# Kernel tuning notes

Measured on AMD Instinct MI355X. Metric: run time of the kernel, lower is better.

## Reference

```python
import jax, jax.numpy as jnp
import numpy as np


def setup_inputs() -> dict:
    key = jax.random.key(0)
    ks = jax.random.split(key, 6)
    B, S, T, E, D = 16, 128, 128, 512, 512  # batch, enc steps, dec steps, enc units, dec units
    scale = 0.05
    return {
        "enc": jax.random.normal(ks[0], (B, S, E), dtype=jnp.float32),
        "dec": jax.random.normal(ks[1], (B, T, D), dtype=jnp.float32),
        "W1": jax.random.normal(ks[2], (E, E), dtype=jnp.float32) * scale,
        "W2": jax.random.normal(ks[3], (D, E), dtype=jnp.float32) * scale,
        "b": jax.random.normal(ks[4], (1, 1, E), dtype=jnp.float32) * scale,
        "V": jax.random.normal(ks[5], (E, 1), dtype=jnp.float32) * scale,
    }


def reference(enc, dec, W1, W2, b, V):
    # Vectorized Bahdanau additive attention (the original loops over decoder
    # timesteps with keras.backend.rnn; the steps are independent so we batch them).
    W1_hs = jnp.einsum('bse,ef->bsf', enc, W1)            # [B,S,E] (computed once, not per step)
    W2_ht = jnp.einsum('btd,de->bte', dec, W2)            # [B,T,E]
    # tanh(W1.hs + W2.ht + b): broadcast to [B,T,S,E]
    scores = jnp.tanh(W1_hs[:, None, :, :] + W2_ht[:, :, None, :] + b)
    logits = jnp.einsum('btse,e->bts', scores, V[:, 0])   # [B,T,S]
    attn_weights = jax.nn.softmax(logits, axis=-1)        # softmax over encoder steps
    context_vectors = jnp.einsum('bts,bse->bte', attn_weights, enc)  # [B,T,E]
    return (context_vectors, attn_weights)
```

## Files before the change

kernel.cpp:

```cpp
#include <hip/hip_runtime.h>
#include <hip/hip_bf16.h>
#include <cstddef>


constexpr int nBt = 16, nSq = 128, nTq = 128, nEd = 512;

typedef __attribute__((ext_vector_type(4))) float f32x4;
typedef __attribute__((ext_vector_type(8))) short s16x8;

#define PRESCALE 2.8853900817779268f
#define LOG2E 1.4426950408889634f

__device__ __forceinline__ unsigned short to_bf(float f) {
    unsigned u = __builtin_bit_cast(unsigned, f);
    return (unsigned short)((u + 0x7FFFu + ((u >> 16) & 1u)) >> 16);
}
__device__ __forceinline__ float from_bf(unsigned short h) {
    unsigned u = ((unsigned)h) << 16;
    return __builtin_bit_cast(float, u);
}

__global__ __launch_bounds__(256) void kWprep(
    const float* __restrict__ W1, const float* __restrict__ W2,
    unsigned short* __restrict__ WT)
{
    const int z = blockIdx.z;
    const float* W = z ? W2 : W1;
    __shared__ float tl[32][33];
    const int r  = threadIdx.x >> 3;
    const int c4 = (threadIdx.x & 7) * 4;
    const int kB = blockIdx.y * 32;
    const int nB = blockIdx.x * 32;
    const float4 v = *(const float4*)&W[(size_t)(kB + r) * nEd + nB + c4];
    tl[r][c4 + 0] = v.x; tl[r][c4 + 1] = v.y;
    tl[r][c4 + 2] = v.z; tl[r][c4 + 3] = v.w;
    __syncthreads();
    unsigned short hh[4], ll[4];
    #pragma unroll
    for (int i = 0; i < 4; ++i) {
        const float x = tl[c4 + i][r];
        hh[i] = to_bf(x);
        ll[i] = to_bf(x - from_bf(hh[i]));
    }
    const size_t o = ((size_t)z * nEd + nB + r) * nEd + kB + c4;
    *(ushort4*)&WT[o] = *(ushort4*)hh;
    *(ushort4*)&WT[(size_t)2 * nEd * nEd + o] = *(ushort4*)ll;
}

__global__ __launch_bounds__(256) void kMgemmB(
    const float* __restrict__ A0, const float* __restrict__ A1,
    const unsigned short* __restrict__ WT, const float* __restrict__ bias,
    float* __restrict__ C0, float* __restrict__ C1)
{
    const int z = blockIdx.z;
    const float* __restrict__ A = z ? A1 : A0;
    const unsigned short* __restrict__ Wh = WT + (size_t)z * nEd * nEd;
    const unsigned short* __restrict__ Wl = Wh + (size_t)2 * nEd * nEd;
    float* __restrict__ C = z ? C1 : C0;

    __shared__ unsigned short sAh[32][72];
    __shared__ unsigned short sAl[32][72];
    __shared__ unsigned short sBh[128][72];
    __shared__ unsigned short sBl[128][72];

    const int tid  = threadIdx.x;
    const int lane = tid & 63;
    const int wv   = tid >> 6;
    const int rowB = blockIdx.y * 32;
    const int colB = blockIdx.x * 128;

    const int ar = tid >> 3, ak = (tid & 7) * 8;
    const int br = tid >> 1, bc = (tid & 1) * 32;

    f32x4 acc[2][2] = {};
    const int l15 = lane & 15;
    const int kh  = lane >> 4;

    for (int k0 = 0; k0 < nEd; k0 += 64) {
        const float4 ga0 = *(const float4*)&A[(size_t)(rowB + ar) * nEd + k0 + ak];
        const float4 ga1 = *(const float4*)&A[(size_t)(rowB + ar) * nEd + k0 + ak + 4];
        const size_t wo = (size_t)(colB + br) * nEd + k0 + bc;
        s16x8 gh[4], gl[4];
        #pragma unroll
        for (int j = 0; j < 4; ++j) {
            gh[j] = *(const s16x8*)&Wh[wo + 8 * j];
            gl[j] = *(const s16x8*)&Wl[wo + 8 * j];
        }

        __syncthreads();
        {
            const float a8[8] = {ga0.x, ga0.y, ga0.z, ga0.w,
                                 ga1.x, ga1.y, ga1.z, ga1.w};
            unsigned short h[8], l[8];
            #pragma unroll
            for (int i = 0; i < 8; ++i) {
                h[i] = to_bf(a8[i]);
                l[i] = to_bf(a8[i] - from_bf(h[i]));
            }
            *(ushort4*)&sAh[ar][ak]     = *(ushort4*)&h[0];
            *(ushort4*)&sAh[ar][ak + 4] = *(ushort4*)&h[4];
            *(ushort4*)&sAl[ar][ak]     = *(ushort4*)&l[0];
            *(ushort4*)&sAl[ar][ak + 4] = *(ushort4*)&l[4];
        }
        #pragma unroll
        for (int j = 0; j < 4; ++j) {
            *(s16x8*)&sBh[br][bc + 8 * j] = gh[j];
            *(s16x8*)&sBl[br][bc + 8 * j] = gl[j];
        }
        __syncthreads();

        #pragma unroll
        for (int kk = 0; kk < 2; ++kk) {
            s16x8 fAh[2], fAl[2], fBh[2], fBl[2];
            #pragma unroll
            for (int mi = 0; mi < 2; ++mi) {
                fAh[mi] = *(const s16x8*)&sAh[mi * 16 + l15][kk * 32 + kh * 8];
                fAl[mi] = *(const s16x8*)&sAl[mi * 16 + l15][kk * 32 + kh * 8];
            }
            #pragma unroll
            for (int ni = 0; ni < 2; ++ni) {
                fBh[ni] = *(const s16x8*)&sBh[wv * 32 + ni * 16 + l15][kk * 32 + kh * 8];
                fBl[ni] = *(const s16x8*)&sBl[wv * 32 + ni * 16 + l15][kk * 32 + kh * 8];
            }
            #pragma unroll
            for (int mi = 0; mi < 2; ++mi)
                #pragma unroll
                for (int ni = 0; ni < 2; ++ni) {
                    f32x4 a = acc[mi][ni];
                    a = __builtin_amdgcn_mfma_f32_16x16x32_bf16(fAh[mi], fBh[ni], a, 0, 0, 0);
                    a = __builtin_amdgcn_mfma_f32_16x16x32_bf16(fAl[mi], fBh[ni], a, 0, 0, 0);
                    a = __builtin_amdgcn_mfma_f32_16x16x32_bf16(fAh[mi], fBl[ni], a, 0, 0, 0);
                    acc[mi][ni] = a;
                }
        }
    }

    #pragma unroll
    for (int ni = 0; ni < 2; ++ni) {
        const int col = colB + wv * 32 + ni * 16 + l15;
        const float bval = z ? bias[col] : 0.0f;
        #pragma unroll
        for (int mi = 0; mi < 2; ++mi) {
            #pragma unroll
            for (int r = 0; r < 4; ++r) {
                const int row = rowB + mi * 16 + kh * 4 + r;
                C[(size_t)row * nEd + col] =
                    __builtin_amdgcn_exp2f((acc[mi][ni][r] + bval) * PRESCALE);
            }
        }
    }
}

__global__ __launch_bounds__(256) void kLogits(
    const float* __restrict__ X1e,
    const float* __restrict__ X2e,
    const float* __restrict__ V,
    float* __restrict__ lg)
{
    const int sg = blockIdx.x, tg = blockIdx.y, b = blockIdx.z;
    const int tid  = threadIdx.x;
    const int lane = tid & 63;
    const int w    = tid >> 6;
    const int s0 = sg * 32 + w * 8;
    const int t0 = tg * 4;

    const float4* vp = (const float4*)V;
    const float4  v0 = vp[lane * 2], v1 = vp[lane * 2 + 1];
    const float4 n0 = make_float4(-2.f * v0.x, -2.f * v0.y, -2.f * v0.z, -2.f * v0.w);
    const float4 n1 = make_float4(-2.f * v1.x, -2.f * v1.y, -2.f * v1.z, -2.f * v1.w);
    const float vsum = v0.x + v0.y + v0.z + v0.w + v1.x + v1.y + v1.z + v1.w;

    float4 c0[4], c1[4];
    #pragma unroll
    for (int i = 0; i < 4; ++i) {
        const float4* xp = (const float4*)(X2e + ((size_t)b * nTq + t0 + i) * nEd);
        c0[i] = xp[lane * 2];
        c1[i] = xp[lane * 2 + 1];
    }

    for (int si = 0; si < 8; ++si) {
        const int s = s0 + si;
        const float4* ap = (const float4*)(X1e + ((size_t)b * nSq + s) * nEd);
        const float4 x0 = ap[lane * 2], x1 = ap[lane * 2 + 1];
        float acc[4];
        #pragma unroll
        for (int t = 0; t < 4; ++t) {
            float a = vsum;
            a += n0.x * __builtin_amdgcn_rcpf(x0.x * c0[t].x + 1.0f);
            a += n0.y * __builtin_amdgcn_rcpf(x0.y * c0[t].y + 1.0f);
            a += n0.z * __builtin_amdgcn_rcpf(x0.z * c0[t].z + 1.0f);
            a += n0.w * __builtin_amdgcn_rcpf(x0.w * c0[t].w + 1.0f);
            a += n1.x * __builtin_amdgcn_rcpf(x1.x * c1[t].x + 1.0f);
            a += n1.y * __builtin_amdgcn_rcpf(x1.y * c1[t].y + 1.0f);
            a += n1.z * __builtin_amdgcn_rcpf(x1.z * c1[t].z + 1.0f);
            a += n1.w * __builtin_amdgcn_rcpf(x1.w * c1[t].w + 1.0f);
            acc[t] = a;
        }
        #pragma unroll
        for (int t = 0; t < 4; ++t) {
            float a = acc[t];
            #pragma unroll
            for (int off = 32; off >= 1; off >>= 1)
                a += __shfl_xor(a, off);
            if (lane == 0)
                lg[((size_t)b * nTq + t0 + t) * nSq + s] = a;
        }
    }
}

__global__ __launch_bounds__(256) void kEncT(
    const float* __restrict__ enc, unsigned short* __restrict__ encT)
{
    const int b = blockIdx.z;
    __shared__ float tl[32][33];
    const int r  = threadIdx.x >> 3;
    const int c4 = (threadIdx.x & 7) * 4;
    const int sB = blockIdx.y * 32;
    const int eB = blockIdx.x * 32;
    const float4 v = *(const float4*)&enc[((size_t)b * nSq + sB + r) * nEd + eB + c4];
    tl[r][c4 + 0] = v.x; tl[r][c4 + 1] = v.y;
    tl[r][c4 + 2] = v.z; tl[r][c4 + 3] = v.w;
    __syncthreads();
    unsigned short o[4];
    #pragma unroll
    for (int i = 0; i < 4; ++i) o[i] = to_bf(tl[c4 + i][r]);
    *(ushort4*)&encT[((size_t)b * nEd + eB + r) * nSq + sB + c4] = *(ushort4*)o;
}

__global__ __launch_bounds__(256) void kSoftW(float* __restrict__ attnw)
{
    const int bt = blockIdx.x * 4 + (threadIdx.x >> 6);
    const int lane = threadIdx.x & 63;
    const float l0 = attnw[(size_t)bt * nSq + lane];
    const float l1 = attnw[(size_t)bt * nSq + lane + 64];
    float m = fmaxf(l0, l1);
    #pragma unroll
    for (int off = 32; off >= 1; off >>= 1)
        m = fmaxf(m, __shfl_xor(m, off));
    const float e0 = __builtin_amdgcn_exp2f((l0 - m) * LOG2E);
    const float e1 = __builtin_amdgcn_exp2f((l1 - m) * LOG2E);
    float sum = e0 + e1;
    #pragma unroll
    for (int off = 32; off >= 1; off >>= 1)
        sum += __shfl_xor(sum, off);
    const float inv = __builtin_amdgcn_rcpf(sum);
    attnw[(size_t)bt * nSq + lane]      = e0 * inv;
    attnw[(size_t)bt * nSq + lane + 64] = e1 * inv;
}

__global__ __launch_bounds__(256) void kCtxMM(
    const float* __restrict__ attnw,
    const unsigned short* __restrict__ encT,
    float* __restrict__ ctx)
{
    const int b  = blockIdx.z;
    const int tB = blockIdx.y * 32;
    const int eB = blockIdx.x * 64;

    __shared__ unsigned short sA[32][136];
    __shared__ unsigned short sB[64][136];

    const int tid  = threadIdx.x;
    const int lane = tid & 63;
    const int w    = tid >> 6;
    const int wm = (w >> 1) * 16;
    const int wn = (w & 1) * 32;
    const int l15 = lane & 15;
    const int kh  = lane >> 4;

    {
        const int r = tid >> 3, c = (tid & 7) * 16;
        const float* ap = &attnw[((size_t)b * nTq + tB + r) * nSq + c];
        unsigned short h[16];
        #pragma unroll
        for (int q = 0; q < 4; ++q) {
            const float4 v = *(const float4*)(ap + 4 * q);
            h[4 * q + 0] = to_bf(v.x); h[4 * q + 1] = to_bf(v.y);
            h[4 * q + 2] = to_bf(v.z); h[4 * q + 3] = to_bf(v.w);
        }
        *(s16x8*)&sA[r][c]     = *(s16x8*)&h[0];
        *(s16x8*)&sA[r][c + 8] = *(s16x8*)&h[8];
    }
    {
        const int r = tid >> 2, c = (tid & 3) * 32;
        const size_t o = ((size_t)b * nEd + eB + r) * nSq + c;
        *(s16x8*)&sB[r][c]      = *(const s16x8*)&encT[o];
        *(s16x8*)&sB[r][c + 8]  = *(const s16x8*)&encT[o + 8];
        *(s16x8*)&sB[r][c + 16] = *(const s16x8*)&encT[o + 16];
        *(s16x8*)&sB[r][c + 24] = *(const s16x8*)&encT[o + 24];
    }
    __syncthreads();

    f32x4 acc[2] = {};
    #pragma unroll
    for (int kk = 0; kk < 4; ++kk) {
        const s16x8 fA = *(const s16x8*)&sA[wm + l15][kk * 32 + kh * 8];
        #pragma unroll
        for (int ni = 0; ni < 2; ++ni) {
            const s16x8 fB = *(const s16x8*)&sB[wn + ni * 16 + l15][kk * 32 + kh * 8];
            acc[ni] = __builtin_amdgcn_mfma_f32_16x16x32_bf16(fA, fB, acc[ni], 0, 0, 0);
        }
    }

    #pragma unroll
    for (int ni = 0; ni < 2; ++ni) {
        const int e = eB + wn + ni * 16 + l15;
        #pragma unroll
        for (int r = 0; r < 4; ++r) {
            const int t = tB + wm + kh * 4 + r;
            ctx[((size_t)b * nTq + t) * nEd + e] = acc[ni][r];
        }
    }
}

extern "C" void kernel_launch(void* const* d_in, const int* in_sizes, int n_in,
                              void* d_out, int out_size, void* d_ws, size_t ws_size,
                              hipStream_t stream) {
    const float* enc = (const float*)d_in[0];
    const float* dec = (const float*)d_in[1];
    const float* W1  = (const float*)d_in[2];
    const float* W2  = (const float*)d_in[3];
    const float* bv  = (const float*)d_in[4];
    const float* V   = (const float*)d_in[5];

    float* ctx   = (float*)d_out;
    float* attnw = (float*)d_out + (size_t)nBt * nTq * nEd;

    unsigned short* WT = (unsigned short*)d_out;

    float* ws0 = (float*)d_ws;
    float* ws1 = ws0 + (size_t)nBt * nSq * nEd;
    unsigned short* encT = (unsigned short*)d_ws;

    kWprep<<<dim3(nEd / 32, nEd / 32, 2), dim3(256), 0, stream>>>(W1, W2, WT);
    kMgemmB<<<dim3(nEd / 128, (nBt * nSq) / 32, 2), dim3(256), 0, stream>>>(
        enc, dec, WT, bv, ws0, ws1);
    kLogits<<<dim3(4, 32, nBt), dim3(256), 0, stream>>>(ws0, ws1, V, attnw);
    kEncT<<<dim3(nEd / 32, nSq / 32, nBt), dim3(256), 0, stream>>>(enc, encT);
    kSoftW<<<dim3((nBt * nTq) / 4), dim3(256), 0, stream>>>(attnw);
    kCtxMM<<<dim3(nEd / 64, nTq / 32, nBt), dim3(256), 0, stream>>>(
        attnw, encT, ctx);
}
```

Measured before the change: 58.65 us.

## Fuse weight and encoder prep kernels; pipeline and compact logits reduction

When the workspace is large enough, the weight split/transpose and the encoder transpose now run in one merged kPrep launch. encT is placed after the GEMM outputs so it can be built early, which removes a separate launch. kLogits prefetches the next encoder row while computing the current one, and packs four per-t partial sums across lane bits so fewer cross-lane shuffles are needed. It also drops the constant V-sum term, which softmax cancels. The fallback path keeps the old launch order, which adds some code duplication.

```diff
diff --git a/kernel.cpp b/kernel.cpp
--- a/kernel.cpp
+++ b/kernel.cpp
@@ -20,191 +20,50 @@
     return __builtin_bit_cast(float, u);
 }
 
-__global__ __launch_bounds__(256) void kWprep(
+__global__ __launch_bounds__(256) void kPrep(
     const float* __restrict__ W1, const float* __restrict__ W2,
-    unsigned short* __restrict__ WT)
-{
-    const int z = blockIdx.z;
-    const float* W = z ? W2 : W1;
+    unsigned short* __restrict__ WT,
+    const float* __restrict__ enc, unsigned short* __restrict__ encT)
+{
     __shared__ float tl[32][33];
     const int r  = threadIdx.x >> 3;
     const int c4 = (threadIdx.x & 7) * 4;
-    const int kB = blockIdx.y * 32;
-    const int nB = blockIdx.x * 32;
-    const float4 v = *(const float4*)&W[(size_t)(kB + r) * nEd + nB + c4];
-    tl[r][c4 + 0] = v.x; tl[r][c4 + 1] = v.y;
-    tl[r][c4 + 2] = v.z; tl[r][c4 + 3] = v.w;
-    __syncthreads();
-    unsigned short hh[4], ll[4];
-    #pragma unroll
-    for (int i = 0; i < 4; ++i) {
-        const float x = tl[c4 + i][r];
-        hh[i] = to_bf(x);
-        ll[i] = to_bf(x - from_bf(hh[i]));
-    }
-    const size_t o = ((size_t)z * nEd + nB + r) * nEd + kB + c4;
-    *(ushort4*)&WT[o] = *(ushort4*)hh;
-    *(ushort4*)&WT[(size_t)2 * nEd * nEd + o] = *(ushort4*)ll;
-}
-
-__global__ __launch_bounds__(256) void kMgemmB(
-    const float* __restrict__ A0, const float* __restrict__ A1,
-    const unsigned short* __restrict__ WT, const float* __restrict__ bias,
-    float* __restrict__ C0, float* __restrict__ C1)
-{
-    const int z = blockIdx.z;
-    const float* __restrict__ A = z ? A1 : A0;
-    const unsigned short* __restrict__ Wh = WT + (size_t)z * nEd * nEd;
-    const unsigned short* __restrict__ Wl = Wh + (size_t)2 * nEd * nEd;
-    float* __restrict__ C = z ? C1 : C0;
-
-    __shared__ unsigned short sAh[32][72];
-    __shared__ unsigned short sAl[32][72];
-    __shared__ unsigned short sBh[128][72];
-    __shared__ unsigned short sBl[128][72];
-
-    const int tid  = threadIdx.x;
-    const int lane = tid & 63;
-    const int wv   = tid >> 6;
-    const int rowB = blockIdx.y * 32;
-    const int colB = blockIdx.x * 128;
-
-    const int ar = tid >> 3, ak = (tid & 7) * 8;
-    const int br = tid >> 1, bc = (tid & 1) * 32;
-
-    f32x4 acc[2][2] = {};
-    const int l15 = lane & 15;
-    const int kh  = lane >> 4;
-
-    for (int k0 = 0; k0 < nEd; k0 += 64) {
-        const float4 ga0 = *(const float4*)&A[(size_t)(rowB + ar) * nEd + k0 + ak];
-        const float4 ga1 = *(const float4*)&A[(size_t)(rowB + ar) * nEd + k0 + ak + 4];
-        const size_t wo = (size_t)(colB + br) * nEd + k0 + bc;
-        s16x8 gh[4], gl[4];
-        #pragma unroll
-        for (int j = 0; j < 4; ++j) {
-            gh[j] = *(const s16x8*)&Wh[wo + 8 * j];
-            gl[j] = *(const s16x8*)&Wl[wo + 8 * j];
-        }
-
+    int bid = blockIdx.x;
+
+    if (bid < 512) {
+        const int z = bid >> 8;
+        const int yx = bid & 255;
+        const int kB = (yx >> 4) * 32;
+        const int nB = (yx & 15) * 32;
+        const float* W = z ? W2 : W1;
+        const float4 v = *(const float4*)&W[(size_t)(kB + r) * nEd + nB + c4];
+        tl[r][c4 + 0] = v.x; tl[r][c4 + 1] = v.y;
+        tl[r][c4 + 2] = v.z; tl[r][c4 + 3] = v.w;
         __syncthreads();
-        {
-            const float a8[8] = {ga0.x, ga0.y, ga0.z, ga0.w,
-                                 ga1.x, ga1.y, ga1.z, ga1.w};
-            unsigned short h[8], l[8];
-            #pragma unroll
-            for (int i = 0; i < 8; ++i) {
-                h[i] = to_bf(a8[i]);
-                l[i] = to_bf(a8[i] - from_bf(h[i]));
-            }
-            *(ushort4*)&sAh[ar][ak]     = *(ushort4*)&h[0];
-            *(ushort4*)&sAh[ar][ak + 4] = *(ushort4*)&h[4];
-            *(ushort4*)&sAl[ar][ak]     = *(ushort4*)&l[0];
-            *(ushort4*)&sAl[ar][ak + 4] = *(ushort4*)&l[4];
-        }
-        #pragma unroll
-        for (int j = 0; j < 4; ++j) {
-            *(s16x8*)&sBh[br][bc + 8 * j] = gh[j];
-            *(s16x8*)&sBl[br][bc + 8 * j] = gl[j];
-        }
+        unsigned short hh[4], ll[4];
+        #pragma unroll
+        for (int i = 0; i < 4; ++i) {
+            const float x = tl[c4 + i][r];
+            hh[i] = to_bf(x);
+            ll[i] = to_bf(x - from_bf(hh[i]));
+        }
+        const size_t o = ((size_t)z * nEd + nB + r) * nEd + kB + c4;
+        *(ushort4*)&WT[o] = *(ushort4*)hh;
+        *(ushort4*)&WT[(size_t)2 * nEd * nEd + o] = *(ushort4*)ll;
+    } else {
+        bid -= 512;
+        const int b = bid >> 6;
+        const int r6 = bid & 63;
+        const int eB = (r6 & 15) * 32;
+        const int sB = (r6 >> 4) * 32;
+        const float4 v = *(const float4*)&enc[((size_t)b * nSq + sB + r) * nEd + eB + c4];
+        tl[r][c4 + 0] = v.x; tl[r][c4 + 1] = v.y;
+        tl[r][c4 + 2] = v.z; tl[r][c4 + 3] = v.w;
         __syncthreads();
-
-        #pragma unroll
-        for (int kk = 0; kk < 2; ++kk) {
-            s16x8 fAh[2], fAl[2], fBh[2], fBl[2];
-            #pragma unroll
-            for (int mi = 0; mi < 2; ++mi) {
-                fAh[mi] = *(const s16x8*)&sAh[mi * 16 + l15][kk * 32 + kh * 8];
-                fAl[mi] = *(const s16x8*)&sAl[mi * 16 + l15][kk * 32 + kh * 8];
-            }
-            #pragma unroll
-            for (int ni = 0; ni < 2; ++ni) {
-                fBh[ni] = *(const s16x8*)&sBh[wv * 32 + ni * 16 + l15][kk * 32 + kh * 8];
-                fBl[ni] = *(const s16x8*)&sBl[wv * 32 + ni * 16 + l15][kk * 32 + kh * 8];
-            }
-            #pragma unroll
-            for (int mi = 0; mi < 2; ++mi)
-                #pragma unroll
-                for (int ni = 0; ni < 2; ++ni) {
-                    f32x4 a = acc[mi][ni];
-                    a = __builtin_amdgcn_mfma_f32_16x16x32_bf16(fAh[mi], fBh[ni], a, 0, 0, 0);
-                    a = __builtin_amdgcn_mfma_f32_16x16x32_bf16(fAl[mi], fBh[ni], a, 0, 0, 0);
-                    a = __builtin_amdgcn_mfma_f32_16x16x32_bf16(fAh[mi], fBl[ni], a, 0, 0, 0);
-                    acc[mi][ni] = a;
-                }
-        }
-    }
-
-    #pragma unroll
-    for (int ni = 0; ni < 2; ++ni) {
-        const int col = colB + wv * 32 + ni * 16 + l15;
-        const float bval = z ? bias[col] : 0.0f;
-        #pragma unroll
-        for (int mi = 0; mi < 2; ++mi) {
-            #pragma unroll
-            for (int r = 0; r < 4; ++r) {
-                const int row = rowB + mi * 16 + kh * 4 + r;
-                C[(size_t)row * nEd + col] =
-                    __builtin_amdgcn_exp2f((acc[mi][ni][r] + bval) * PRESCALE);
-            }
-        }
-    }
-}
-
-__global__ __launch_bounds__(256) void kLogits(
-    const float* __restrict__ X1e,
-    const float* __restrict__ X2e,
-    const float* __restrict__ V,
-    float* __restrict__ lg)
-{
-    const int sg = blockIdx.x, tg = blockIdx.y, b = blockIdx.z;
-    const int tid  = threadIdx.x;
-    const int lane = tid & 63;
-    const int w    = tid >> 6;
-    const int s0 = sg * 32 + w * 8;
-    const int t0 = tg * 4;
-
-    const float4* vp = (const float4*)V;
-    const float4  v0 = vp[lane * 2], v1 = vp[lane * 2 + 1];
-    const float4 n0 = make_float4(-2.f * v0.x, -2.f * v0.y, -2.f * v0.z, -2.f * v0.w);
-    const float4 n1 = make_float4(-2.f * v1.x, -2.f * v1.y, -2.f * v1.z, -2.f * v1.w);
-    const float vsum = v0.x + v0.y + v0.z + v0.w + v1.x + v1.y + v1.z + v1.w;
-
-    float4 c0[4], c1[4];
-    #pragma unroll
-    for (int i = 0; i < 4; ++i) {
-        const float4* xp = (const float4*)(X2e + ((size_t)b * nTq + t0 + i) * nEd);
-        c0[i] = xp[lane * 2];
-        c1[i] = xp[lane * 2 + 1];
-    }
-
-    for (int si = 0; si < 8; ++si) {
-        const int s = s0 + si;
-        const float4* ap = (const float4*)(X1e + ((size_t)b * nSq + s) * nEd);
-        const float4 x0 = ap[lane * 2], x1 = ap[lane * 2 + 1];
-        float acc[4];
-        #pragma unroll
-        for (int t = 0; t < 4; ++t) {
-            float a = vsum;
-            a += n0.x * __builtin_amdgcn_rcpf(x0.x * c0[t].x + 1.0f);
-            a += n0.y * __builtin_amdgcn_rcpf(x0.y * c0[t].y + 1.0f);
-            a += n0.z * __builtin_amdgcn_rcpf(x0.z * c0[t].z + 1.0f);
-            a += n0.w * __builtin_amdgcn_rcpf(x0.w * c0[t].w + 1.0f);
-            a += n1.x * __builtin_amdgcn_rcpf(x1.x * c1[t].x + 1.0f);
-            a += n1.y * __builtin_amdgcn_rcpf(x1.y * c1[t].y + 1.0f);
-            a += n1.z * __builtin_amdgcn_rcpf(x1.z * c1[t].z + 1.0f);
-            a += n1.w * __builtin_amdgcn_rcpf(x1.w * c1[t].w + 1.0f);
-            acc[t] = a;
-        }
-        #pragma unroll
-        for (int t = 0; t < 4; ++t) {
-            float a = acc[t];
-            #pragma unroll
-            for (int off = 32; off >= 1; off >>= 1)
-                a += __shfl_xor(a, off);
-            if (lane == 0)
-                lg[((size_t)b * nTq + t0 + t) * nSq + s] = a;
-        }
+        unsigned short o[4];
+        #pragma unroll
+        for (int i = 0; i < 4; ++i) o[i] = to_bf(tl[c4 + i][r]);
+        *(ushort4*)&encT[((size_t)b * nEd + eB + r) * nSq + sB + c4] = *(ushort4*)o;
     }
 }
 
@@ -227,6 +86,180 @@
     *(ushort4*)&encT[((size_t)b * nEd + eB + r) * nSq + sB + c4] = *(ushort4*)o;
 }
 
+__global__ __launch_bounds__(256) void kMgemmB(
+    const float* __restrict__ A0, const float* __restrict__ A1,
+    const unsigned short* __restrict__ WT, const float* __restrict__ bias,
+    float* __restrict__ C0, float* __restrict__ C1)
+{
+    const int z = blockIdx.z;
+    const float* __restrict__ A = z ? A1 : A0;
+    const unsigned short* __restrict__ Wh = WT + (size_t)z * nEd * nEd;
+    const unsigned short* __restrict__ Wl = Wh + (size_t)2 * nEd * nEd;
+    float* __restrict__ C = z ? C1 : C0;
+
+    __shared__ unsigned short sAh[32][72];
+    __shared__ unsigned short sAl[32][72];
+    __shared__ unsigned short sBh[128][72];
+    __shared__ unsigned short sBl[128][72];
+
+    const int tid  = threadIdx.x;
+    const int lane = tid & 63;
+    const int wv   = tid >> 6;
+    const int rowB = blockIdx.y * 32;
+    const int colB = blockIdx.x * 128;
+
+    const int ar = tid >> 3, ak = (tid & 7) * 8;
+    const int br = tid >> 1, bc = (tid & 1) * 32;
+
+    f32x4 acc[2][2] = {};
+    const int l15 = lane & 15;
+    const int kh  = lane >> 4;
+
+    for (int k0 = 0; k0 < nEd; k0 += 64) {
+        const float4 ga0 = *(const float4*)&A[(size_t)(rowB + ar) * nEd + k0 + ak];
+        const float4 ga1 = *(const float4*)&A[(size_t)(rowB + ar) * nEd + k0 + ak + 4];
+        const size_t wo = (size_t)(colB + br) * nEd + k0 + bc;
+        s16x8 gh[4], gl[4];
+        #pragma unroll
+        for (int j = 0; j < 4; ++j) {
+            gh[j] = *(const s16x8*)&Wh[wo + 8 * j];
+            gl[j] = *(const s16x8*)&Wl[wo + 8 * j];
+        }
+
+        __syncthreads();
+        {
+            const float a8[8] = {ga0.x, ga0.y, ga0.z, ga0.w,
+                                 ga1.x, ga1.y, ga1.z, ga1.w};
+            unsigned short h[8], l[8];
+            #pragma unroll
+            for (int i = 0; i < 8; ++i) {
+                h[i] = to_bf(a8[i]);
+                l[i] = to_bf(a8[i] - from_bf(h[i]));
+            }
+            *(ushort4*)&sAh[ar][ak]     = *(ushort4*)&h[0];
+            *(ushort4*)&sAh[ar][ak + 4] = *(ushort4*)&h[4];
+            *(ushort4*)&sAl[ar][ak]     = *(ushort4*)&l[0];
+            *(ushort4*)&sAl[ar][ak + 4] = *(ushort4*)&l[4];
+        }
+        #pragma unroll
+        for (int j = 0; j < 4; ++j) {
+            *(s16x8*)&sBh[br][bc + 8 * j] = gh[j];
+            *(s16x8*)&sBl[br][bc + 8 * j] = gl[j];
+        }
+        __syncthreads();
+
+        #pragma unroll
+        for (int kk = 0; kk < 2; ++kk) {
+            s16x8 fAh[2], fAl[2], fBh[2], fBl[2];
+            #pragma unroll
+            for (int mi = 0; mi < 2; ++mi) {
+                fAh[mi] = *(const s16x8*)&sAh[mi * 16 + l15][kk * 32 + kh * 8];
+                fAl[mi] = *(const s16x8*)&sAl[mi * 16 + l15][kk * 32 + kh * 8];
+            }
+            #pragma unroll
+            for (int ni = 0; ni < 2; ++ni) {
+                fBh[ni] = *(const s16x8*)&sBh[wv * 32 + ni * 16 + l15][kk * 32 + kh * 8];
+                fBl[ni] = *(const s16x8*)&sBl[wv * 32 + ni * 16 + l15][kk * 32 + kh * 8];
+            }
+            #pragma unroll
+            for (int mi = 0; mi < 2; ++mi)
+                #pragma unroll
+                for (int ni = 0; ni < 2; ++ni) {
+                    f32x4 a = acc[mi][ni];
+                    a = __builtin_amdgcn_mfma_f32_16x16x32_bf16(fAh[mi], fBh[ni], a, 0, 0, 0);
+                    a = __builtin_amdgcn_mfma_f32_16x16x32_bf16(fAl[mi], fBh[ni], a, 0, 0, 0);
+                    a = __builtin_amdgcn_mfma_f32_16x16x32_bf16(fAh[mi], fBl[ni], a, 0, 0, 0);
+                    acc[mi][ni] = a;
+                }
+        }
+    }
+
+    #pragma unroll
+    for (int ni = 0; ni < 2; ++ni) {
+        const int col = colB + wv * 32 + ni * 16 + l15;
+        const float bval = z ? bias[col] : 0.0f;
+        #pragma unroll
+        for (int mi = 0; mi < 2; ++mi) {
+            #pragma unroll
+            for (int r = 0; r < 4; ++r) {
+                const int row = rowB + mi * 16 + kh * 4 + r;
+                C[(size_t)row * nEd + col] =
+                    __builtin_amdgcn_exp2f((acc[mi][ni][r] + bval) * PRESCALE);
+            }
+        }
+    }
+}
+
+__global__ __launch_bounds__(256) void kLogits(
+    const float* __restrict__ X1e,
+    const float* __restrict__ X2e,
+    const float* __restrict__ V,
+    float* __restrict__ lg)
+{
+    const int sg = blockIdx.x, tg = blockIdx.y, b = blockIdx.z;
+    const int tid  = threadIdx.x;
+    const int lane = tid & 63;
+    const int w    = tid >> 6;
+    const int s0 = sg * 32 + w * 8;
+    const int t0 = tg * 4;
+
+    const float4* vp = (const float4*)V;
+    const float4  v0 = vp[lane * 2], v1 = vp[lane * 2 + 1];
+    const float4 n0 = make_float4(-2.f * v0.x, -2.f * v0.y, -2.f * v0.z, -2.f * v0.w);
+    const float4 n1 = make_float4(-2.f * v1.x, -2.f * v1.y, -2.f * v1.z, -2.f * v1.w);
+
+    float4 c0[4], c1[4];
+    #pragma unroll
+    for (int i = 0; i < 4; ++i) {
+        const float4* xp = (const float4*)(X2e + ((size_t)b * nTq + t0 + i) * nEd);
+        c0[i] = xp[lane * 2];
+        c1[i] = xp[lane * 2 + 1];
+    }
+
+    const float* X1b = X1e + (size_t)b * nSq * nEd;
+    float4 x0 = ((const float4*)(X1b + (size_t)s0 * nEd))[lane * 2];
+    float4 x1 = ((const float4*)(X1b + (size_t)s0 * nEd))[lane * 2 + 1];
+
+    #pragma unroll
+    for (int si = 0; si < 8; ++si) {
+        const float4 cx0 = x0, cx1 = x1;
+        if (si < 7) {
+            const float4* np = (const float4*)(X1b + (size_t)(s0 + si + 1) * nEd);
+            x0 = np[lane * 2];
+            x1 = np[lane * 2 + 1];
+        }
+        float acc[4];
+        #pragma unroll
+        for (int t = 0; t < 4; ++t) {
+            float a;
+            a  = n0.x * __builtin_amdgcn_rcpf(cx0.x * c0[t].x + 1.0f);
+            a += n0.y * __builtin_amdgcn_rcpf(cx0.y * c0[t].y + 1.0f);
+            a += n0.z * __builtin_amdgcn_rcpf(cx0.z * c0[t].z + 1.0f);
+            a += n0.w * __builtin_amdgcn_rcpf(cx0.w * c0[t].w + 1.0f);
+            a += n1.x * __builtin_amdgcn_rcpf(cx1.x * c1[t].x + 1.0f);
+            a += n1.y * __builtin_amdgcn_rcpf(cx1.y * c1[t].y + 1.0f);
+            a += n1.z * __builtin_amdgcn_rcpf(cx1.z * c1[t].z + 1.0f);
+            a += n1.w * __builtin_amdgcn_rcpf(cx1.w * c1[t].w + 1.0f);
+            acc[t] = a;
+        }
+        float t01a = acc[0] + __shfl_xor(acc[0], 1);
+        float t01b = acc[1] + __shfl_xor(acc[1], 1);
+        float a01  = (lane & 1) ? t01b : t01a;
+        float t23a = acc[2] + __shfl_xor(acc[2], 1);
+        float t23b = acc[3] + __shfl_xor(acc[3], 1);
+        float a23  = (lane & 1) ? t23b : t23a;
+        float q01 = a01 + __shfl_xor(a01, 2);
+        float q23 = a23 + __shfl_xor(a23, 2);
+        float q = (lane & 2) ? q23 : q01;
+        q += __shfl_xor(q, 4);
+        q += __shfl_xor(q, 8);
+        q += __shfl_xor(q, 16);
+        q += __shfl_xor(q, 32);
+        if (lane < 4)
+            lg[((size_t)b * nTq + t0 + lane) * nSq + s0 + si] = q;
+    }
+}
+
 __global__ __launch_bounds__(256) void kSoftW(float* __restrict__ attnw)
 {
     const int bt = blockIdx.x * 4 + (threadIdx.x >> 6);
@@ -330,13 +363,25 @@
 
     float* ws0 = (float*)d_ws;
     float* ws1 = ws0 + (size_t)nBt * nSq * nEd;
-    unsigned short* encT = (unsigned short*)d_ws;
-
-    kWprep<<<dim3(nEd / 32, nEd / 32, 2), dim3(256), 0, stream>>>(W1, W2, WT);
-    kMgemmB<<<dim3(nEd / 128, (nBt * nSq) / 32, 2), dim3(256), 0, stream>>>(
-        enc, dec, WT, bv, ws0, ws1);
-    kLogits<<<dim3(4, 32, nBt), dim3(256), 0, stream>>>(ws0, ws1, V, attnw);
-    kEncT<<<dim3(nEd / 32, nSq / 32, nBt), dim3(256), 0, stream>>>(enc, encT);
+
+    const size_t eight_mb = (size_t)8 * 1024 * 1024;
+    const bool early = ws_size >= eight_mb + (size_t)2 * 1024 * 1024 + 4096;
+    unsigned short* encT = early
+        ? (unsigned short*)((char*)d_ws + eight_mb)
+        : (unsigned short*)d_ws;
+
+    if (early) {
+        kPrep<<<dim3(1536), dim3(256), 0, stream>>>(W1, W2, WT, enc, encT);
+        kMgemmB<<<dim3(nEd / 128, (nBt * nSq) / 32, 2), dim3(256), 0, stream>>>(
+            enc, dec, WT, bv, ws0, ws1);
+        kLogits<<<dim3(4, 32, nBt), dim3(256), 0, stream>>>(ws0, ws1, V, attnw);
+    } else {
+        kPrep<<<dim3(512), dim3(256), 0, stream>>>(W1, W2, WT, enc, encT);
+        kMgemmB<<<dim3(nEd / 128, (nBt * nSq) / 32, 2), dim3(256), 0, stream>>>(
+            enc, dec, WT, bv, ws0, ws1);
+        kLogits<<<dim3(4, 32, nBt), dim3(256), 0, stream>>>(ws0, ws1, V, attnw);
+        kEncT<<<dim3(nEd / 32, nSq / 32, nBt), dim3(256), 0, stream>>>(enc, encT);
+    }
     kSoftW<<<dim3((nBt * nTq) / 4), dim3(256), 0, stream>>>(attnw);
     kCtxMM<<<dim3(nEd / 64, nTq / 32, nBt), dim3(256), 0, stream>>>(
         attnw, encT, ctx);
```

Result: faster. 52.33 us (-10.8%).
